# Kernel optimization log

Hardware: AMD Instinct MI355X
Metric: run time of the kernel (lower is better)

## Reference

```python
import jax, jax.numpy as jnp
import numpy as np

E = 2048
H = 16
D = E // H  # head_dim = 128
S_SLOTS = 8
EPS = 1e-5


def _linear_params(key, fan_in, fan_out):
    kw, kb = jax.random.split(key)
    lim = 1.0 / np.sqrt(fan_in)
    W = jax.random.uniform(kw, (fan_out, fan_in), jnp.float32, -lim, lim)
    b = jax.random.uniform(kb, (fan_out,), jnp.float32, -lim, lim)
    return W, b


def setup_inputs() -> dict:
    key = jax.random.key(0)
    ks = jax.random.split(key, 10)
    x = jax.random.normal(ks[0], (2, 2048, E), jnp.float32)
    thought_slots = jax.random.normal(ks[1], (S_SLOTS, E), jnp.float32)
    Wq, bq = _linear_params(ks[2], E, E)
    Wk, bk = _linear_params(ks[3], E, E)
    Wv, bv = _linear_params(ks[4], E, E)
    Wtq, btq = _linear_params(ks[5], E, E)
    Wtk, btk = _linear_params(ks[6], E, E)
    Wtv, btv = _linear_params(ks[7], E, E)
    Wo, bo = _linear_params(ks[8], E, E)
    gamma = jnp.ones((E,), jnp.float32)
    beta = jnp.zeros((E,), jnp.float32)
    return dict(x=x, thought_slots=thought_slots, Wq=Wq, bq=bq, Wk=Wk, bk=bk,
                Wv=Wv, bv=bv, Wtq=Wtq, btq=btq, Wtk=Wtk, btk=btk,
                Wtv=Wtv, btv=btv, Wo=Wo, bo=bo, gamma=gamma, beta=beta)


def _heads(t, B):
    # [B, S, E] -> [B, H, S, D]
    return t.reshape(B, -1, H, D).transpose(0, 2, 1, 3)


def reference(x, thought_slots, Wq, bq, Wk, bk, Wv, bv,
              Wtq, btq, Wtk, btk, Wtv, btv, Wo, bo, gamma, beta):
    B, S, _ = x.shape
    scale = 1.0 / np.sqrt(D)

    # regular self-attention stream
    q = _heads(x @ Wq.T + bq, B)
    k = _heads(x @ Wk.T + bk, B)
    v = _heads(x @ Wv.T + bv, B)
    attn = jax.nn.softmax(jnp.einsum('bhqd,bhkd->bhqk', q, k) * scale, axis=-1)
    regular_out = jnp.einsum('bhqk,bhkd->bhqd', attn, v)

    # thought cross-attention stream (keys/values from learned slots)
    slots = jnp.broadcast_to(thought_slots, (B, S_SLOTS, thought_slots.shape[-1]))
    t_q = _heads(x @ Wtq.T + btq, B)
    t_k = _heads(slots @ Wtk.T + btk, B)
    t_v = _heads(slots @ Wtv.T + btv, B)
    t_attn = jax.nn.softmax(jnp.einsum('bhqd,bhkd->bhqk', t_q, t_k) * scale, axis=-1)
    thought_out = jnp.einsum('bhqk,bhkd->bhqd', t_attn, t_v)

    # merge heads, combine, layernorm, output projection
    combined = (regular_out + thought_out).transpose(0, 2, 1, 3).reshape(B, S, E)
    mu = jnp.mean(combined, axis=-1, keepdims=True)
    var = jnp.var(combined, axis=-1, keepdims=True)
    normed = (combined - mu) * jax.lax.rsqrt(var + EPS) * gamma + beta
    return normed @ Wo.T + bo
```

## Files before the change

kernel.cpp:

```cpp
#include <hip/hip_runtime.h>
#include <hip/hip_bf16.h>
#include <stdint.h>

typedef __bf16 bf16;
typedef __bf16 bf16x8 __attribute__((ext_vector_type(8)));
typedef __bf16 bf16x4 __attribute__((ext_vector_type(4)));
typedef float f32x4 __attribute__((ext_vector_type(4)));

#define E_DIM 2048
#define HEADS 16
#define HD 128
#define SEQ 2048
#define BATCH 2
#define NTOK 4096
#define NSLOT 8

#define QSCALE (0.08838834764831845f * 1.4426950408889634f)

__device__ __forceinline__ void gload_lds16(const void* g, void* lds) {
  __builtin_amdgcn_global_load_lds(
      (const __attribute__((address_space(1))) uint32_t*)g,
      (__attribute__((address_space(3))) uint32_t*)lds, 16, 0, 0);
}

__global__ __launch_bounds__(256) void cvt_f32_bf16_kernel(
    const float* __restrict__ src, bf16* __restrict__ dst, int n8)
{
  for (int i = blockIdx.x * 256 + threadIdx.x; i < n8; i += gridDim.x * 256) {
    const f32x4 a = *(const f32x4*)(src + i * 8);
    const f32x4 b = *(const f32x4*)(src + i * 8 + 4);
    bf16x8 o;
#pragma unroll
    for (int j = 0; j < 4; j++) { o[j] = (bf16)a[j]; o[4 + j] = (bf16)b[j]; }
    *(bf16x8*)(dst + i * 8) = o;
  }
}

struct ProjArgs {
  const bf16* W[4];
  const float* bias[4];
  void* out[4];
  int mode[4];
  float scale[4];
};

__global__ __launch_bounds__(256) void gemm_nt_kernel(
    const bf16* __restrict__ A, ProjArgs pa, int M, int N, int K)
{
  __shared__ bf16 As[2][128 * 32];
  __shared__ bf16 Bs[2][128 * 32];

  const int z = blockIdx.z;
  const bf16* __restrict__ W = pa.W[z];
  const float* __restrict__ bias = pa.bias[z];
  void* __restrict__ out = pa.out[z];
  const int mode = pa.mode[z];
  const float scale = pa.scale[z];

  const int tid = threadIdx.x;
  const int lane = tid & 63;
  const int w = tid >> 6;
  const int wr = w >> 1, wc = w & 1;
  const int g = lane >> 4, c = lane & 15;
  const int bm = blockIdx.x, bn = blockIdx.y;

  f32x4 acc[4][4] = {};

  const int srow = lane >> 2;
  const int scol = (lane & 3) * 8;
  const bf16* Ab = A + (size_t)(bm * 128 + srow) * K + scol;
  const bf16* Wb = W + (size_t)(bn * 128 + srow) * K + scol;

  auto stage = [&](int k0, int buf) {
#pragma unroll
    for (int i = 0; i < 2; ++i) {
      const int chunk = w * 2 + i;
      gload_lds16(Ab + (size_t)(chunk * 16) * K + k0, (char*)(&As[buf][0]) + chunk * 1024);
      gload_lds16(Wb + (size_t)(chunk * 16) * K + k0, (char*)(&Bs[buf][0]) + chunk * 1024);
    }
  };

  stage(0, 0);
  __syncthreads();
  int cur = 0;

  for (int k0 = 0; k0 < K; k0 += 32) {
    if (k0 + 32 < K) stage(k0 + 32, cur ^ 1);
    bf16x8 af[4], bfr[4];
#pragma unroll
    for (int m = 0; m < 4; m++)
      af[m] = *(const bf16x8*)(&As[cur][0] + (wr * 64 + m * 16 + c) * 32 + g * 8);
#pragma unroll
    for (int n = 0; n < 4; n++)
      bfr[n] = *(const bf16x8*)(&Bs[cur][0] + (wc * 64 + n * 16 + c) * 32 + g * 8);
#pragma unroll
    for (int m = 0; m < 4; m++)
#pragma unroll
      for (int n = 0; n < 4; n++)
        acc[m][n] = __builtin_amdgcn_mfma_f32_16x16x32_bf16(af[m], bfr[n], acc[m][n], 0, 0, 0);
    __syncthreads();
    cur ^= 1;
  }

#pragma unroll
  for (int m = 0; m < 4; m++) {
#pragma unroll
    for (int n = 0; n < 4; n++) {
      const int col = bn * 128 + wc * 64 + n * 16 + c;
      const float bv = bias[col];
#pragma unroll
      for (int j = 0; j < 4; j++) {
        const int row = bm * 128 + wr * 64 + m * 16 + g * 4 + j;
        const float v = (acc[m][n][j] + bv) * scale;
        if (mode == 0) {
          ((float*)out)[(size_t)row * N + col] = v;
        } else {
          const int b = row >> 11, s = row & 2047;
          const int h = col >> 7, d = col & 127;
          size_t idx;
          if (mode == 1) idx = (((size_t)(b * HEADS + h)) * SEQ + s) * HD + d;
          else           idx = (((size_t)(b * HEADS + h)) * HD + d) * SEQ + s;
          ((bf16*)out)[idx] = (bf16)v;
        }
      }
    }
  }
}

__global__ __launch_bounds__(256) void slots_proj_kernel(
    const float* __restrict__ slots,
    const float* __restrict__ Wk, const float* __restrict__ bk,
    const float* __restrict__ Wv, const float* __restrict__ bv,
    float* __restrict__ tk, float* __restrict__ tv)
{
  const int col = blockIdx.x * 256 + threadIdx.x;
  const int slot = blockIdx.y;
  const int mat = blockIdx.z;
  const float* W = mat ? Wv : Wk;
  const float* bias = mat ? bv : bk;
  float* out = mat ? tv : tk;
  const float* xr = slots + (size_t)slot * E_DIM;
  const float* wr = W + (size_t)col * E_DIM;
  float acc = 0.f;
  for (int k = 0; k < E_DIM; k += 4) {
    const f32x4 a = *(const f32x4*)(xr + k);
    const f32x4 b4 = *(const f32x4*)(wr + k);
#pragma unroll
    for (int i = 0; i < 4; i++) acc += a[i] * b4[i];
  }
  out[(size_t)slot * E_DIM + col] = acc + bias[col];
}

__global__ __launch_bounds__(256) void flash_attn_kernel(
    const bf16* __restrict__ Qg, const bf16* __restrict__ Kg,
    const bf16* __restrict__ Vtg, bf16* __restrict__ Og)
{
  __shared__ char Ks[2][64 * 256];
  __shared__ char Vs[2][128 * 128];
  __shared__ char Ps[4][4096];

  const int orig = blockIdx.x;
  const int logical = (orig & 7) * 64 + (orig >> 3);
  const int qt = logical & 15;
  const int bh = logical >> 4;

  const int tid = threadIdx.x;
  const int lane = tid & 63;
  const int w = tid >> 6;
  const int g = lane >> 4, c = lane & 15;
  const int b = bh >> 4, h = bh & 15;
  const int q0 = qt * 128 + w * 32;

  const bf16* Qb = Qg + ((size_t)bh * SEQ + q0) * HD;
  const bf16* Kb = Kg + (size_t)bh * SEQ * HD;
  const bf16* Vb = Vtg + (size_t)bh * HD * SEQ;
  char* Pw = Ps[w];

  auto stage = [&](int kv0, int buf) {
#pragma unroll
    for (int i = 0; i < 4; i++) {
      const int chunk = w * 4 + i;
      const int p = chunk * 1024 + lane * 16;
      {
        const int r = p >> 8;
        const int sl = ((p >> 4) & 15) ^ (r & 7);
        gload_lds16(Kb + (size_t)(kv0 + r) * HD + sl * 8, &Ks[buf][0] + chunk * 1024);
      }
      {
        const int r = p >> 7;
        const int sl = ((p >> 4) & 7) ^ (r & 7);
        gload_lds16(Vb + (size_t)r * SEQ + kv0 + sl * 8, &Vs[buf][0] + chunk * 1024);
      }
    }
  };

  bf16x8 qf[4][2];
#pragma unroll
  for (int kk = 0; kk < 4; kk++)
#pragma unroll
    for (int n = 0; n < 2; n++)
      qf[kk][n] = *(const bf16x8*)(Qb + (size_t)(n * 16 + c) * HD + kk * 32 + g * 8);

  stage(0, 0);
  __syncthreads();
  int cur = 0;

  f32x4 acc[2][8] = {};
  float mrun[2] = {-1e30f, -1e30f};
  float lrun[2] = {0.f, 0.f};

  for (int kv0 = 0; kv0 < SEQ; kv0 += 64) {
    if (kv0 + 64 < SEQ) stage(kv0 + 64, cur ^ 1);

    f32x4 st[4][2] = {};
#pragma unroll
    for (int kk = 0; kk < 4; kk++) {
      bf16x8 kf[4];
#pragma unroll
      for (int kfr = 0; kfr < 4; kfr++) {
        const int r = kfr * 16 + c;
        const int sl = (kk * 4 + g) ^ (r & 7);
        kf[kfr] = *(const bf16x8*)(&Ks[cur][0] + r * 256 + sl * 16);
      }
      __builtin_amdgcn_s_setprio(1);
#pragma unroll
      for (int kfr = 0; kfr < 4; kfr++)
#pragma unroll
        for (int n = 0; n < 2; n++)
          st[kfr][n] = __builtin_amdgcn_mfma_f32_16x16x32_bf16(kf[kfr], qf[kk][n], st[kfr][n], 0, 0, 0);
      __builtin_amdgcn_s_setprio(0);
    }

    float fsc[2];
#pragma unroll
    for (int n = 0; n < 2; n++) {
      float lm = -1e30f;
#pragma unroll
      for (int kfr = 0; kfr < 4; kfr++)
#pragma unroll
        for (int j = 0; j < 4; j++) lm = fmaxf(lm, st[kfr][n][j]);
      lm = fmaxf(lm, __shfl_xor(lm, 16));
      lm = fmaxf(lm, __shfl_xor(lm, 32));
      const float mn = fmaxf(mrun[n], lm);
      fsc[n] = exp2f(mrun[n] - mn);
      mrun[n] = mn;
      float ps = 0.f;
#pragma unroll
      for (int kfr = 0; kfr < 4; kfr++)
#pragma unroll
        for (int j = 0; j < 4; j++) {
          const float pp = exp2f(st[kfr][n][j] - mn);
          st[kfr][n][j] = pp;
          ps += pp;
        }
      ps += __shfl_xor(ps, 16);
      ps += __shfl_xor(ps, 32);
      lrun[n] = lrun[n] * fsc[n] + ps;
    }

#pragma unroll
    for (int m = 0; m < 2; m++)
#pragma unroll
      for (int j = 0; j < 4; j++) {
        const float fj = __shfl(fsc[m], (lane & 48) | (g * 4 + j));
#pragma unroll
        for (int n = 0; n < 8; n++) acc[m][n][j] *= fj;
      }

#pragma unroll
    for (int n = 0; n < 2; n++)
#pragma unroll
      for (int kfr = 0; kfr < 4; kfr++) {
        bf16x4 pk;
#pragma unroll
        for (int j = 0; j < 4; j++) pk[j] = (bf16)st[kfr][n][j];
        const int q = n * 16 + c;
        const int L = q * 128 + kfr * 32 + g * 8;
        *(bf16x4*)(Pw + (L ^ ((q & 7) << 4))) = pk;
      }

#pragma unroll
    for (int kk = 0; kk < 2; kk++) {
      bf16x8 pf[2];
#pragma unroll
      for (int m = 0; m < 2; m++) {
        const int q = m * 16 + c;
        const int L = q * 128 + kk * 64 + g * 16;
        pf[m] = *(const bf16x8*)(Pw + (L ^ ((q & 7) << 4)));
      }
      __builtin_amdgcn_s_setprio(1);
#pragma unroll
      for (int n = 0; n < 8; n++) {
        const int d = n * 16 + c;
        const int Lv = d * 128 + kk * 64 + g * 16;
        const bf16x8 vf = *(const bf16x8*)(&Vs[cur][0] + (Lv ^ ((d & 7) << 4)));
#pragma unroll
        for (int m = 0; m < 2; m++)
          acc[m][n] = __builtin_amdgcn_mfma_f32_16x16x32_bf16(pf[m], vf, acc[m][n], 0, 0, 0);
      }
      __builtin_amdgcn_s_setprio(0);
    }

    __syncthreads();
    cur ^= 1;
  }

#pragma unroll
  for (int m = 0; m < 2; m++) {
#pragma unroll
    for (int j = 0; j < 4; j++) {
      const float lb = __shfl(lrun[m], (lane & 48) | (g * 4 + j));
      const float linv = 1.0f / lb;
      const int s = q0 + m * 16 + g * 4 + j;
#pragma unroll
      for (int n = 0; n < 8; n++) {
        const int e = h * HD + n * 16 + c;
        Og[((size_t)b * SEQ + s) * E_DIM + e] = (bf16)(acc[m][n][j] * linv);
      }
    }
  }
}

__global__ __launch_bounds__(256) void thought_ln_kernel(
    const bf16* __restrict__ TQ, const float* __restrict__ TK,
    const float* __restrict__ TV, const bf16* __restrict__ ATT,
    const float* __restrict__ gamma, const float* __restrict__ beta,
    bf16* __restrict__ Y)
{
  __shared__ float wsum[4], wsq[4];
  const int tid = threadIdx.x;
  const int lane = tid & 63;
  const int w = tid >> 6;
  const int tok = blockIdx.x;
  const int b = tok >> 11, s = tok & 2047;
  const int e0 = tid * 8;
  const int h = e0 >> 7;
  const int d0 = e0 & 127;

  const bf16x8 av = *(const bf16x8*)(ATT + (size_t)tok * E_DIM + e0);
  float v[8];
#pragma unroll
  for (int i = 0; i < 8; i++) v[i] = (float)av[i];

  const bf16x8 qv8 = *(const bf16x8*)(TQ + (((size_t)(b * HEADS + h)) * SEQ + s) * HD + d0);
  float qv[8];
#pragma unroll
  for (int i = 0; i < 8; i++) qv[i] = (float)qv8[i];

  float dts[NSLOT];
#pragma unroll
  for (int sl = 0; sl < NSLOT; sl++) {
    const float* tkr = TK + (size_t)sl * E_DIM + e0;
    const f32x4 k0 = *(const f32x4*)(tkr);
    const f32x4 k1 = *(const f32x4*)(tkr + 4);
    float dp = 0.f;
#pragma unroll
    for (int i = 0; i < 4; i++) dp += qv[i] * k0[i] + qv[4 + i] * k1[i];
    dp += __shfl_xor(dp, 1);
    dp += __shfl_xor(dp, 2);
    dp += __shfl_xor(dp, 4);
    dp += __shfl_xor(dp, 8);
    dts[sl] = dp;
  }
  float mx = dts[0];
#pragma unroll
  for (int sl = 1; sl < NSLOT; sl++) mx = fmaxf(mx, dts[sl]);
  float p[NSLOT], den = 0.f;
#pragma unroll
  for (int sl = 0; sl < NSLOT; sl++) { p[sl] = exp2f(dts[sl] - mx); den += p[sl]; }
  const float dinv = 1.0f / den;
#pragma unroll
  for (int sl = 0; sl < NSLOT; sl++) {
    const float pn = p[sl] * dinv;
    const float* tvr = TV + (size_t)sl * E_DIM + e0;
    const f32x4 v0 = *(const f32x4*)(tvr);
    const f32x4 v1 = *(const f32x4*)(tvr + 4);
#pragma unroll
    for (int i = 0; i < 4; i++) { v[i] += pn * v0[i]; v[4 + i] += pn * v1[i]; }
  }

  float sm = 0.f, sq = 0.f;
#pragma unroll
  for (int i = 0; i < 8; i++) { sm += v[i]; sq += v[i] * v[i]; }
#pragma unroll
  for (int d = 1; d < 64; d <<= 1) { sm += __shfl_xor(sm, d); sq += __shfl_xor(sq, d); }
  if (lane == 0) { wsum[w] = sm; wsq[w] = sq; }
  __syncthreads();
  const float ts = wsum[0] + wsum[1] + wsum[2] + wsum[3];
  const float tq2 = wsq[0] + wsq[1] + wsq[2] + wsq[3];
  const float mean = ts * (1.f / E_DIM);
  const float var = tq2 * (1.f / E_DIM) - mean * mean;
  const float rstd = rsqrtf(var + 1e-5f);
  const f32x4 g0 = *(const f32x4*)(gamma + e0);
  const f32x4 g1 = *(const f32x4*)(gamma + e0 + 4);
  const f32x4 b0 = *(const f32x4*)(beta + e0);
  const f32x4 b1 = *(const f32x4*)(beta + e0 + 4);
  bf16x8 outv;
#pragma unroll
  for (int i = 0; i < 4; i++) {
    outv[i]     = (bf16)((v[i]     - mean) * rstd * g0[i] + b0[i]);
    outv[4 + i] = (bf16)((v[4 + i] - mean) * rstd * g1[i] + b1[i]);
  }
  *(bf16x8*)(Y + (size_t)tok * E_DIM + e0) = outv;
}

extern "C" void kernel_launch(void* const* d_in, const int* in_sizes, int n_in,
                              void* d_out, int out_size, void* d_ws, size_t ws_size,
                              hipStream_t stream) {
  (void)in_sizes; (void)n_in; (void)out_size; (void)ws_size;
  const float* x     = (const float*)d_in[0];
  const float* slots = (const float*)d_in[1];
  const float* Wq  = (const float*)d_in[2];   const float* bq  = (const float*)d_in[3];
  const float* Wk  = (const float*)d_in[4];   const float* bk  = (const float*)d_in[5];
  const float* Wv  = (const float*)d_in[6];   const float* bv  = (const float*)d_in[7];
  const float* Wtq = (const float*)d_in[8];   const float* btq = (const float*)d_in[9];
  const float* Wtk = (const float*)d_in[10];  const float* btk = (const float*)d_in[11];
  const float* Wtv = (const float*)d_in[12];  const float* btv = (const float*)d_in[13];
  const float* Wo  = (const float*)d_in[14];  const float* bo  = (const float*)d_in[15];
  const float* gamma = (const float*)d_in[16];
  const float* beta  = (const float*)d_in[17];

  uint8_t* ws = (uint8_t*)d_ws;
  const size_t BUF  = (size_t)NTOK * E_DIM * sizeof(bf16);
  const size_t WBUF = (size_t)E_DIM * E_DIM * sizeof(bf16);
  bf16* xb   = (bf16*)(ws + 0 * BUF);
  bf16* qb   = (bf16*)(ws + 1 * BUF);
  bf16* kb   = (bf16*)(ws + 2 * BUF);
  bf16* vtb  = (bf16*)(ws + 3 * BUF);
  bf16* tqb  = (bf16*)(ws + 4 * BUF);
  bf16* attb = (bf16*)(ws + 5 * BUF);
  bf16* nrmb = qb;
  uint8_t* wp = ws + 6 * BUF;
  bf16* Wqb  = (bf16*)(wp + 0 * WBUF);
  bf16* Wkb  = (bf16*)(wp + 1 * WBUF);
  bf16* Wvb  = (bf16*)(wp + 2 * WBUF);
  bf16* Wtqb = (bf16*)(wp + 3 * WBUF);
  bf16* Wob  = (bf16*)(wp + 4 * WBUF);
  float* tkb = (float*)(wp + 5 * WBUF);
  float* tvb = (float*)(wp + 5 * WBUF + 128 * 1024);

  const int WN8 = E_DIM * E_DIM / 8;
  const int XN8 = NTOK * E_DIM / 8;
  cvt_f32_bf16_kernel<<<dim3(2048), 256, 0, stream>>>(x, xb, XN8);
  cvt_f32_bf16_kernel<<<dim3(1024), 256, 0, stream>>>(Wq, Wqb, WN8);
  cvt_f32_bf16_kernel<<<dim3(1024), 256, 0, stream>>>(Wk, Wkb, WN8);
  cvt_f32_bf16_kernel<<<dim3(1024), 256, 0, stream>>>(Wv, Wvb, WN8);
  cvt_f32_bf16_kernel<<<dim3(1024), 256, 0, stream>>>(Wtq, Wtqb, WN8);
  cvt_f32_bf16_kernel<<<dim3(1024), 256, 0, stream>>>(Wo, Wob, WN8);

  ProjArgs pa;
  pa.W[0] = Wqb;  pa.bias[0] = bq;  pa.out[0] = qb;  pa.mode[0] = 1; pa.scale[0] = QSCALE;
  pa.W[1] = Wkb;  pa.bias[1] = bk;  pa.out[1] = kb;  pa.mode[1] = 1; pa.scale[1] = 1.0f;
  pa.W[2] = Wvb;  pa.bias[2] = bv;  pa.out[2] = vtb; pa.mode[2] = 2; pa.scale[2] = 1.0f;
  pa.W[3] = Wtqb; pa.bias[3] = btq; pa.out[3] = tqb; pa.mode[3] = 1; pa.scale[3] = QSCALE;
  gemm_nt_kernel<<<dim3(NTOK / 128, E_DIM / 128, 4), 256, 0, stream>>>(
      xb, pa, NTOK, E_DIM, E_DIM);

  slots_proj_kernel<<<dim3(E_DIM / 256, NSLOT, 2), 256, 0, stream>>>(
      slots, Wtk, btk, Wtv, btv, tkb, tvb);

  flash_attn_kernel<<<dim3((SEQ / 128) * BATCH * HEADS), 256, 0, stream>>>(
      qb, kb, vtb, attb);
  thought_ln_kernel<<<dim3(NTOK), 256, 0, stream>>>(
      tqb, tkb, tvb, attb, gamma, beta, nrmb);

  ProjArgs po;
  po.W[0] = Wob; po.bias[0] = bo; po.out[0] = d_out; po.mode[0] = 0; po.scale[0] = 1.0f;
  po.W[1] = po.W[2] = po.W[3] = Wob;
  po.bias[1] = po.bias[2] = po.bias[3] = bo;
  po.out[1] = po.out[2] = po.out[3] = d_out;
  po.mode[1] = po.mode[2] = po.mode[3] = 0;
  po.scale[1] = po.scale[2] = po.scale[3] = 1.0f;
  gemm_nt_kernel<<<dim3(NTOK / 128, E_DIM / 128, 1), 256, 0, stream>>>(
      nrmb, po, NTOK, E_DIM, E_DIM);
}
```

Before: 528.7 us.

## Use 256x256 GEMM tiles with swizzled LDS and lazy flash rescaling

Replaces the 128x128x32 projection GEMM with a 256x256x64 tile kernel using 512 threads. It XOR-swizzles the LDS layout to avoid bank conflicts and remaps workgroups so neighbouring blocks spread across XCD chiplets. Separately, flash attention now updates the running max and rescales the accumulator only when some row's max grows by more than 8 in log2 space, which skips most rescale multiplies. The larger tiles use 128 KB of LDS per block, which lowers occupancy, and the 128-block output GEMM leaves some CUs idle.

```diff
diff --git a/kernel.cpp b/kernel.cpp
--- a/kernel.cpp
+++ b/kernel.cpp
@@ -44,13 +44,20 @@
   float scale[4];
 };
 
-__global__ __launch_bounds__(256) void gemm_nt_kernel(
-    const bf16* __restrict__ A, ProjArgs pa, int M, int N, int K)
+__global__ __launch_bounds__(512, 2) void gemm256_kernel(
+    const bf16* __restrict__ A, ProjArgs pa, int nbm, int nbn)
 {
-  __shared__ bf16 As[2][128 * 32];
-  __shared__ bf16 Bs[2][128 * 32];
-
-  const int z = blockIdx.z;
+  __shared__ bf16 As[2][256 * 64];
+  __shared__ bf16 Bs[2][256 * 64];
+
+  const int nwg = gridDim.x;
+  const int qch = nwg >> 3;
+  const int wg = (blockIdx.x & 7) * qch + (blockIdx.x >> 3);
+  const int bm = wg % nbm;
+  const int rest = wg / nbm;
+  const int bn = rest % nbn;
+  const int z = rest / nbn;
+
   const bf16* __restrict__ W = pa.W[z];
   const float* __restrict__ bias = pa.bias[z];
   void* __restrict__ out = pa.out[z];
@@ -60,60 +67,78 @@
   const int tid = threadIdx.x;
   const int lane = tid & 63;
   const int w = tid >> 6;
-  const int wr = w >> 1, wc = w & 1;
+  const int wr = w >> 2;
+  const int wc = w & 3;
   const int g = lane >> 4, c = lane & 15;
-  const int bm = blockIdx.x, bn = blockIdx.y;
-
-  f32x4 acc[4][4] = {};
-
-  const int srow = lane >> 2;
-  const int scol = (lane & 3) * 8;
-  const bf16* Ab = A + (size_t)(bm * 128 + srow) * K + scol;
-  const bf16* Wb = W + (size_t)(bn * 128 + srow) * K + scol;
-
-  auto stage = [&](int k0, int buf) {
-#pragma unroll
-    for (int i = 0; i < 2; ++i) {
-      const int chunk = w * 2 + i;
-      gload_lds16(Ab + (size_t)(chunk * 16) * K + k0, (char*)(&As[buf][0]) + chunk * 1024);
-      gload_lds16(Wb + (size_t)(chunk * 16) * K + k0, (char*)(&Bs[buf][0]) + chunk * 1024);
+
+  const int rsub = lane >> 3;
+  const int csub = ((lane & 7) ^ rsub) * 8;
+
+  const int arow0 = wr * 128 + wc * 32;
+  const int hb = wc >> 1, gj = (wr << 1) | (wc & 1);
+  const int brow0 = hb * 128 + gj * 32;
+  const bf16* Asrc = A + (size_t)(bm * 256 + arow0 + rsub) * 2048 + csub;
+  const bf16* Bsrc = W + (size_t)(bn * 256 + brow0 + rsub) * 2048 + csub;
+
+  auto stage = [&](int t, int buf) {
+    const int k0 = t * 64;
+    char* Adst = (char*)(&As[buf][0]) + arow0 * 128;
+    char* Bdst = (char*)(&Bs[buf][0]) + brow0 * 128;
+#pragma unroll
+    for (int i = 0; i < 4; i++) {
+      gload_lds16(Asrc + (size_t)(i * 8) * 2048 + k0, Adst + i * 1024);
+      gload_lds16(Bsrc + (size_t)(i * 8) * 2048 + k0, Bdst + i * 1024);
     }
   };
+
+  f32x4 acc[8][4] = {};
 
   stage(0, 0);
   __syncthreads();
   int cur = 0;
 
-  for (int k0 = 0; k0 < K; k0 += 32) {
-    if (k0 + 32 < K) stage(k0 + 32, cur ^ 1);
-    bf16x8 af[4], bfr[4];
-#pragma unroll
-    for (int m = 0; m < 4; m++)
-      af[m] = *(const bf16x8*)(&As[cur][0] + (wr * 64 + m * 16 + c) * 32 + g * 8);
-#pragma unroll
-    for (int n = 0; n < 4; n++)
-      bfr[n] = *(const bf16x8*)(&Bs[cur][0] + (wc * 64 + n * 16 + c) * 32 + g * 8);
-#pragma unroll
-    for (int m = 0; m < 4; m++)
-#pragma unroll
-      for (int n = 0; n < 4; n++)
-        acc[m][n] = __builtin_amdgcn_mfma_f32_16x16x32_bf16(af[m], bfr[n], acc[m][n], 0, 0, 0);
+  const int NT = 2048 / 64;
+  for (int t = 0; t < NT; t++) {
+    if (t + 1 < NT) stage(t + 1, cur ^ 1);
+#pragma unroll
+    for (int kk = 0; kk < 2; kk++) {
+      bf16x8 bfr[4], af[8];
+#pragma unroll
+      for (int n = 0; n < 4; n++) {
+        const int row = wc * 64 + n * 16 + c;
+        bfr[n] = *(const bf16x8*)((const char*)(&Bs[cur][0]) + row * 128 +
+                                  (((kk * 4 + g) ^ (c & 7)) * 16));
+      }
+#pragma unroll
+      for (int mi = 0; mi < 8; mi++) {
+        const int row = wr * 128 + mi * 16 + c;
+        af[mi] = *(const bf16x8*)((const char*)(&As[cur][0]) + row * 128 +
+                                  (((kk * 4 + g) ^ (c & 7)) * 16));
+      }
+      __builtin_amdgcn_s_setprio(1);
+#pragma unroll
+      for (int mi = 0; mi < 8; mi++)
+#pragma unroll
+        for (int n = 0; n < 4; n++)
+          acc[mi][n] = __builtin_amdgcn_mfma_f32_16x16x32_bf16(af[mi], bfr[n], acc[mi][n], 0, 0, 0);
+      __builtin_amdgcn_s_setprio(0);
+    }
     __syncthreads();
     cur ^= 1;
   }
 
 #pragma unroll
-  for (int m = 0; m < 4; m++) {
+  for (int mi = 0; mi < 8; mi++) {
 #pragma unroll
     for (int n = 0; n < 4; n++) {
-      const int col = bn * 128 + wc * 64 + n * 16 + c;
+      const int col = bn * 256 + wc * 64 + n * 16 + c;
       const float bv = bias[col];
 #pragma unroll
       for (int j = 0; j < 4; j++) {
-        const int row = bm * 128 + wr * 64 + m * 16 + g * 4 + j;
-        const float v = (acc[m][n][j] + bv) * scale;
+        const int row = bm * 256 + wr * 128 + mi * 16 + g * 4 + j;
+        const float v = (acc[mi][n][j] + bv) * scale;
         if (mode == 0) {
-          ((float*)out)[(size_t)row * N + col] = v;
+          ((float*)out)[(size_t)row * E_DIM + col] = v;
         } else {
           const int b = row >> 11, s = row & 2047;
           const int h = col >> 7, d = col & 127;
@@ -232,6 +257,7 @@
     }
 
     float fsc[2];
+    bool anyresc = false;
 #pragma unroll
     for (int n = 0; n < 2; n++) {
       float lm = -1e30f;
@@ -241,15 +267,20 @@
         for (int j = 0; j < 4; j++) lm = fmaxf(lm, st[kfr][n][j]);
       lm = fmaxf(lm, __shfl_xor(lm, 16));
       lm = fmaxf(lm, __shfl_xor(lm, 32));
-      const float mn = fmaxf(mrun[n], lm);
-      fsc[n] = exp2f(mrun[n] - mn);
-      mrun[n] = mn;
+      if (__any(lm > mrun[n] + 8.0f)) {
+        const float mn = fmaxf(mrun[n], lm);
+        fsc[n] = exp2f(mrun[n] - mn);
+        mrun[n] = mn;
+        anyresc = true;
+      } else {
+        fsc[n] = 1.0f;
+      }
       float ps = 0.f;
 #pragma unroll
       for (int kfr = 0; kfr < 4; kfr++)
 #pragma unroll
         for (int j = 0; j < 4; j++) {
-          const float pp = exp2f(st[kfr][n][j] - mn);
+          const float pp = exp2f(st[kfr][n][j] - mrun[n]);
           st[kfr][n][j] = pp;
           ps += pp;
         }
@@ -258,14 +289,16 @@
       lrun[n] = lrun[n] * fsc[n] + ps;
     }
 
-#pragma unroll
-    for (int m = 0; m < 2; m++)
-#pragma unroll
-      for (int j = 0; j < 4; j++) {
-        const float fj = __shfl(fsc[m], (lane & 48) | (g * 4 + j));
-#pragma unroll
-        for (int n = 0; n < 8; n++) acc[m][n][j] *= fj;
-      }
+    if (anyresc) {
+#pragma unroll
+      for (int m = 0; m < 2; m++)
+#pragma unroll
+        for (int j = 0; j < 4; j++) {
+          const float fj = __shfl(fsc[m], (lane & 48) | (g * 4 + j));
+#pragma unroll
+          for (int n = 0; n < 8; n++) acc[m][n][j] *= fj;
+        }
+    }
 
 #pragma unroll
     for (int n = 0; n < 2; n++)
@@ -453,8 +486,7 @@
   pa.W[1] = Wkb;  pa.bias[1] = bk;  pa.out[1] = kb;  pa.mode[1] = 1; pa.scale[1] = 1.0f;
   pa.W[2] = Wvb;  pa.bias[2] = bv;  pa.out[2] = vtb; pa.mode[2] = 2; pa.scale[2] = 1.0f;
   pa.W[3] = Wtqb; pa.bias[3] = btq; pa.out[3] = tqb; pa.mode[3] = 1; pa.scale[3] = QSCALE;
-  gemm_nt_kernel<<<dim3(NTOK / 128, E_DIM / 128, 4), 256, 0, stream>>>(
-      xb, pa, NTOK, E_DIM, E_DIM);
+  gemm256_kernel<<<dim3(16 * 8 * 4), 512, 0, stream>>>(xb, pa, 16, 8);
 
   slots_proj_kernel<<<dim3(E_DIM / 256, NSLOT, 2), 256, 0, stream>>>(
       slots, Wtk, btk, Wtv, btv, tkb, tvb);
@@ -471,6 +503,5 @@
   po.out[1] = po.out[2] = po.out[3] = d_out;
   po.mode[1] = po.mode[2] = po.mode[3] = 0;
   po.scale[1] = po.scale[2] = po.scale[3] = 1.0f;
-  gemm_nt_kernel<<<dim3(NTOK / 128, E_DIM / 128, 1), 256, 0, stream>>>(
-      nrmb, po, NTOK, E_DIM, E_DIM);
-}
+  gemm256_kernel<<<dim3(16 * 8 * 1), 512, 0, stream>>>(nrmb, po, 16, 8);
+}
```

New measurement: 539.8 us. 1.02x slower.
